# Optimization experiments

Hardware: AMD Instinct MI355X
Metric: run time of the kernel (lower is better)

Reference implementation:

```python
import jax, jax.numpy as jnp
import numpy as np

EPS = 1e-6
TEMP = 1.0
L = 64  # shapelet_len


def _znorm(a):
    # z-normalize over last axis, population std, clamped by EPS (matches torch unbiased=False + clamp_min)
    mean = a.mean(axis=-1, keepdims=True)
    std = jnp.maximum(a.std(axis=-1, keepdims=True), EPS)
    return (a - mean) / std


def setup_inputs() -> dict:
    key = jax.random.key(0)
    k1, k2 = jax.random.split(key)
    bs, T, C, P = 32, 8192, 1, 64
    x = jax.random.normal(k1, (bs, T, C), dtype=jnp.float32)
    shapelets = jax.random.normal(k2, (P, C, L), dtype=jnp.float32)
    return {"x": x, "shapelets": shapelets}


def reference(x, shapelets):
    # x: [bs, T, C]; shapelets: [P, C, L]
    bs, T, C = x.shape
    P = shapelets.shape[0]
    x_ct = jnp.transpose(x, (0, 2, 1))  # [bs, C, T]
    Tp = T - L + 1
    # sliding windows: [bs, C, T', L]
    idx = jnp.arange(Tp)[:, None] + jnp.arange(L)[None, :]
    w = x_ct[:, :, idx]
    # z-normalize windows and shapelets over the length axis
    w = _znorm(w)
    s = _znorm(shapelets)
    # squared euclidean distance via expansion ||w||^2 - 2 w.s + ||s||^2 (sum over C and L)
    w2 = jnp.sum(w * w, axis=(1, 3))          # [bs, T']
    s2 = jnp.sum(s * s, axis=(1, 2))          # [P]
    dot = jnp.einsum('bctl,pcl->btp', w, s)   # [bs, T', P]
    dist2 = w2[:, :, None] + s2[None, None, :] - 2.0 * dot
    temp = max(TEMP, EPS)
    act = jnp.exp(-dist2 / temp)              # [bs, T', P]
    # center-pad to length T: left = L//2, right = T - (T' + left)
    left = L // 2
    right = max(0, T - (Tp + left))
    act_full = jnp.pad(act, ((0, 0), (left, right), (0, 0)))
    return act_full[:, :T, :]
```

## Files before the change

### kernel.cpp

```cpp
#include <hip/hip_runtime.h>
#include <math.h>

#define T_LEN 8192
#define EPSF  1e-6f

typedef __attribute__((ext_vector_type(8))) short short8;
typedef __attribute__((ext_vector_type(4))) float float4v;

__global__ __launch_bounds__(256, 4) void shapelet_fused(
        const float* __restrict__ x,
        const float* __restrict__ sh,
        float* __restrict__ out) {
    __shared__ short8 BfragH[8][64];
    __shared__ short8 BfragL[8][64];
    __shared__ __align__(16) float xs[320];
    __shared__ float4 lstat[256];
    __shared__ __align__(16) float lsum[64];
    __shared__ __align__(16) float ls2[64];

    const int tid  = threadIdx.x;
    const int lane = tid & 63;
    const int wave = tid >> 6;
    const int n    = lane & 15;
    const int quad = lane >> 4;

    const int super = blockIdx.x & 31;
    const int b     = blockIdx.x >> 5;
    const int t0    = super << 8;

    if (tid < 64) {
        const int p = tid;
        const int pt_p = p & 3;
        const int n_p  = p >> 2;

        float S[64];
        const float4* s4 = (const float4*)(sh + (size_t)p * 64);
#pragma unroll
        for (int i = 0; i < 16; ++i) {
            float4 v = s4[i];
            S[4 * i + 0] = v.x;
            S[4 * i + 1] = v.y;
            S[4 * i + 2] = v.z;
            S[4 * i + 3] = v.w;
        }

        float s1 = 0.f;
#pragma unroll
        for (int l = 0; l < 64; ++l) s1 += S[l];
        float mu = s1 * (1.f / 64.f);
        float sq = 0.f;
#pragma unroll
        for (int l = 0; l < 64; ++l) { float d = S[l] - mu; sq = fmaf(d, d, sq); }
        float sd  = fmaxf(sqrtf(sq * (1.f / 64.f)), EPSF);
        float inv = 1.f / sd;
        float ssum = 0.f, ss2 = 0.f;

        unsigned* BH = (unsigned*)BfragH;
        unsigned* BL = (unsigned*)BfragL;
#pragma unroll
        for (int l2 = 0; l2 < 32; ++l2) {
            const int k = 2 * l2;
            unsigned pk_h, pk_l;
            {
                float v = S[k];
                float s = (v - mu) * inv;
                unsigned ub = __float_as_uint(s);
                float hi = __uint_as_float(ub & 0xFFFF0000u);
                float lo = s - hi;
                unsigned lb = __float_as_uint(lo) & 0xFFFF0000u;
                pk_h = ub >> 16;
                pk_l = lb >> 16;
                float eff = hi + __uint_as_float(lb);
                ssum += eff;
                ss2  = fmaf(eff, eff, ss2);
            }
            {
                float v = S[k + 1];
                float s = (v - mu) * inv;
                unsigned ub = __float_as_uint(s);
                float hi = __uint_as_float(ub & 0xFFFF0000u);
                float lo = s - hi;
                unsigned lb = __float_as_uint(lo) & 0xFFFF0000u;
                pk_h |= (ub & 0xFFFF0000u);
                pk_l |= lb;
                float eff = hi + __uint_as_float(lb);
                ssum += eff;
                ss2  = fmaf(eff, eff, ss2);
            }
            const int f  = (pt_p << 1) + (k >> 5);
            const int li = (((k >> 3) & 3) << 4) + n_p;
            const int di = (((f << 6) + li) << 2) + ((k & 7) >> 1);
            BH[di] = pk_h;
            BL[di] = pk_l;
        }
        lsum[p] = ssum;
        ls2[p]  = ss2;
    } else if (tid < 144) {
        const int i = tid - 64;
        int g0 = t0 - 32 + (i << 2);
        float4 v;
        if (g0 >= 0 && g0 + 3 < T_LEN) {
            v = *(const float4*)(x + (size_t)b * T_LEN + g0);
        } else {
            float* vp = (float*)&v;
#pragma unroll
            for (int e = 0; e < 4; ++e) {
                int g = g0 + e;
                vp[e] = ((unsigned)g < (unsigned)T_LEN) ? x[(size_t)b * T_LEN + g] : 0.f;
            }
        }
        *(float4*)&xs[i << 2] = v;
    }
    __syncthreads();

    {
        const int r = tid;
        float s1 = 0.f, sq = 0.f;
#pragma unroll
        for (int l = 0; l < 64; ++l) {
            float v = xs[r + l];
            s1 += v; sq = fmaf(v, v, sq);
        }
        float mu  = s1 * (1.f / 64.f);
        float var = fmaxf(sq * (1.f / 64.f) - mu * mu, 0.f);
        float sd  = fmaxf(sqrtf(var), EPSF);
        float inv = 1.f / sd;
        float4 st;
        st.x = mu;
        st.y = inv;
        st.z = 64.f * var * inv * inv;
        st.w = 0.f;
        lstat[r] = st;
    }
    const float4 sm4 = *(const float4*)&lsum[n << 2];
    const float4 sv4 = *(const float4*)&ls2[n << 2];
    __syncthreads();

    const short8* BH8 = (const short8*)BfragH;
    const short8* BL8 = (const short8*)BfragL;

#pragma unroll
    for (int u = 0; u < 4; ++u) {
        const int abase = (u << 6) + (wave << 4) + n + (quad << 3);
        short8 Ah[2], Al[2];
#pragma unroll
        for (int h = 0; h < 2; ++h) {
#pragma unroll
            for (int j = 0; j < 8; ++j) {
                float v = xs[abase + h * 32 + j];
                unsigned ub = __float_as_uint(v);
                unsigned hb = ub & 0xFFFF0000u;
                float lo = v - __uint_as_float(hb);
                Ah[h][j] = (short)(ub >> 16);
                Al[h][j] = (short)(__float_as_uint(lo) >> 16);
            }
        }

        float4v acc[4];
#pragma unroll
        for (int pt = 0; pt < 4; ++pt) {
            unsigned off = ((unsigned)(pt << 1) << 6) + (unsigned)lane;
            asm volatile("" : "+v"(off));
            short8 bh0 = BH8[off];
            short8 bh1 = BH8[off + 64];
            short8 bl0 = BL8[off];
            short8 bl1 = BL8[off + 64];

            float4v a = {0.f, 0.f, 0.f, 0.f};
            a = __builtin_amdgcn_mfma_f32_16x16x32_bf16(Ah[0], bh0, a, 0, 0, 0);
            a = __builtin_amdgcn_mfma_f32_16x16x32_bf16(Ah[0], bl0, a, 0, 0, 0);
            a = __builtin_amdgcn_mfma_f32_16x16x32_bf16(Al[0], bh0, a, 0, 0, 0);
            a = __builtin_amdgcn_mfma_f32_16x16x32_bf16(Ah[1], bh1, a, 0, 0, 0);
            a = __builtin_amdgcn_mfma_f32_16x16x32_bf16(Ah[1], bl1, a, 0, 0, 0);
            a = __builtin_amdgcn_mfma_f32_16x16x32_bf16(Al[1], bh1, a, 0, 0, 0);
            acc[pt] = a;
        }

#pragma unroll
        for (int r = 0; r < 4; ++r) {
            int tl = (u << 6) + (wave << 4) + (quad << 2) + r;
            int tg = t0 + tl;
            bool valid = (tg >= 32) && (tg <= 8160);
            float4 st = lstat[tl];
            float mu  = st.x;
            float inv = st.y;
            float w2  = st.z;
            float d0 = (acc[0][r] - mu * sm4.x) * inv;
            float d1 = (acc[1][r] - mu * sm4.y) * inv;
            float d2 = (acc[2][r] - mu * sm4.z) * inv;
            float d3 = (acc[3][r] - mu * sm4.w) * inv;
            float4 o;
            o.x = valid ? __expf(-(w2 + sv4.x - 2.f * d0)) : 0.f;
            o.y = valid ? __expf(-(w2 + sv4.y - 2.f * d1)) : 0.f;
            o.z = valid ? __expf(-(w2 + sv4.z - 2.f * d2)) : 0.f;
            o.w = valid ? __expf(-(w2 + sv4.w - 2.f * d3)) : 0.f;
            *(float4*)(out + (((size_t)(b * T_LEN + tg)) << 6) + (n << 2)) = o;
        }
    }
}

extern "C" void kernel_launch(void* const* d_in, const int* in_sizes, int n_in,
                              void* d_out, int out_size, void* d_ws, size_t ws_size,
                              hipStream_t stream) {
    const float* x  = (const float*)d_in[0];
    const float* sh = (const float*)d_in[1];
    float* out = (float*)d_out;

    shapelet_fused<<<32 * 32, 256, 0, stream>>>(x, sh, out);
}
```

Before: 83.88 us.

## Halve per-block time tile, double grid, and cut register pressure for occupancy

Each block now covers 128 time steps instead of 256, so the grid doubles to 2048 blocks and the launch bound asks for 8 waves per SIMD. The shapelet prologue rereads global memory instead of keeping a 64-float register array. The A-fragment bf16 split uses perm-based packing, and the MFMA loop is reordered to process one K-half at a time with accumulators held across halves. The goal is lower VGPR use and better latency hiding, at the cost of redoing the shapelet normalization and B-fragment build in twice as many blocks.

```diff
diff --git a/kernel.cpp b/kernel.cpp
--- a/kernel.cpp
+++ b/kernel.cpp
@@ -7,14 +7,14 @@
 typedef __attribute__((ext_vector_type(8))) short short8;
 typedef __attribute__((ext_vector_type(4))) float float4v;
 
-__global__ __launch_bounds__(256, 4) void shapelet_fused(
+__global__ __launch_bounds__(256, 8) void shapelet_fused(
         const float* __restrict__ x,
         const float* __restrict__ sh,
         float* __restrict__ out) {
     __shared__ short8 BfragH[8][64];
     __shared__ short8 BfragL[8][64];
-    __shared__ __align__(16) float xs[320];
-    __shared__ float4 lstat[256];
+    __shared__ __align__(16) float xs[192];
+    __shared__ float4 lstat[128];
     __shared__ __align__(16) float lsum[64];
     __shared__ __align__(16) float ls2[64];
 
@@ -24,78 +24,83 @@
     const int n    = lane & 15;
     const int quad = lane >> 4;
 
-    const int super = blockIdx.x & 31;
-    const int b     = blockIdx.x >> 5;
-    const int t0    = super << 8;
+    const int super = blockIdx.x & 63;
+    const int b     = blockIdx.x >> 6;
+    const int t0    = super << 7;
 
     if (tid < 64) {
         const int p = tid;
         const int pt_p = p & 3;
         const int n_p  = p >> 2;
-
-        float S[64];
         const float4* s4 = (const float4*)(sh + (size_t)p * 64);
+
+        float s1 = 0.f;
 #pragma unroll
         for (int i = 0; i < 16; ++i) {
             float4 v = s4[i];
-            S[4 * i + 0] = v.x;
-            S[4 * i + 1] = v.y;
-            S[4 * i + 2] = v.z;
-            S[4 * i + 3] = v.w;
-        }
-
-        float s1 = 0.f;
-#pragma unroll
-        for (int l = 0; l < 64; ++l) s1 += S[l];
+            s1 += v.x; s1 += v.y; s1 += v.z; s1 += v.w;
+        }
         float mu = s1 * (1.f / 64.f);
+
         float sq = 0.f;
 #pragma unroll
-        for (int l = 0; l < 64; ++l) { float d = S[l] - mu; sq = fmaf(d, d, sq); }
+        for (int i = 0; i < 16; ++i) {
+            float4 v = s4[i];
+            float d0 = v.x - mu; sq = fmaf(d0, d0, sq);
+            float d1 = v.y - mu; sq = fmaf(d1, d1, sq);
+            float d2 = v.z - mu; sq = fmaf(d2, d2, sq);
+            float d3 = v.w - mu; sq = fmaf(d3, d3, sq);
+        }
         float sd  = fmaxf(sqrtf(sq * (1.f / 64.f)), EPSF);
         float inv = 1.f / sd;
+
         float ssum = 0.f, ss2 = 0.f;
-
         unsigned* BH = (unsigned*)BfragH;
         unsigned* BL = (unsigned*)BfragL;
 #pragma unroll
-        for (int l2 = 0; l2 < 32; ++l2) {
-            const int k = 2 * l2;
-            unsigned pk_h, pk_l;
-            {
-                float v = S[k];
-                float s = (v - mu) * inv;
-                unsigned ub = __float_as_uint(s);
-                float hi = __uint_as_float(ub & 0xFFFF0000u);
-                float lo = s - hi;
-                unsigned lb = __float_as_uint(lo) & 0xFFFF0000u;
-                pk_h = ub >> 16;
-                pk_l = lb >> 16;
-                float eff = hi + __uint_as_float(lb);
-                ssum += eff;
-                ss2  = fmaf(eff, eff, ss2);
-            }
-            {
-                float v = S[k + 1];
-                float s = (v - mu) * inv;
-                unsigned ub = __float_as_uint(s);
-                float hi = __uint_as_float(ub & 0xFFFF0000u);
-                float lo = s - hi;
-                unsigned lb = __float_as_uint(lo) & 0xFFFF0000u;
-                pk_h |= (ub & 0xFFFF0000u);
-                pk_l |= lb;
-                float eff = hi + __uint_as_float(lb);
-                ssum += eff;
-                ss2  = fmaf(eff, eff, ss2);
-            }
-            const int f  = (pt_p << 1) + (k >> 5);
-            const int li = (((k >> 3) & 3) << 4) + n_p;
-            const int di = (((f << 6) + li) << 2) + ((k & 7) >> 1);
-            BH[di] = pk_h;
-            BL[di] = pk_l;
+        for (int i = 0; i < 16; ++i) {
+            float4 v4 = s4[i];
+            const float el[4] = { v4.x, v4.y, v4.z, v4.w };
+#pragma unroll
+            for (int half = 0; half < 2; ++half) {
+                const int k = 4 * i + 2 * half;
+                unsigned pk_h, pk_l;
+                {
+                    float v = el[2 * half];
+                    float s = (v - mu) * inv;
+                    unsigned ub = __float_as_uint(s);
+                    float hi = __uint_as_float(ub & 0xFFFF0000u);
+                    float lo = s - hi;
+                    unsigned lb = __float_as_uint(lo) & 0xFFFF0000u;
+                    pk_h = ub >> 16;
+                    pk_l = lb >> 16;
+                    float eff = hi + __uint_as_float(lb);
+                    ssum += eff;
+                    ss2  = fmaf(eff, eff, ss2);
+                }
+                {
+                    float v = el[2 * half + 1];
+                    float s = (v - mu) * inv;
+                    unsigned ub = __float_as_uint(s);
+                    float hi = __uint_as_float(ub & 0xFFFF0000u);
+                    float lo = s - hi;
+                    unsigned lb = __float_as_uint(lo) & 0xFFFF0000u;
+                    pk_h |= (ub & 0xFFFF0000u);
+                    pk_l |= lb;
+                    float eff = hi + __uint_as_float(lb);
+                    ssum += eff;
+                    ss2  = fmaf(eff, eff, ss2);
+                }
+                const int f  = (pt_p << 1) + (k >> 5);
+                const int li = (((k >> 3) & 3) << 4) + n_p;
+                const int di = (((f << 6) + li) << 2) + ((k & 7) >> 1);
+                BH[di] = pk_h;
+                BL[di] = pk_l;
+            }
         }
         lsum[p] = ssum;
         ls2[p]  = ss2;
-    } else if (tid < 144) {
+    } else if (tid < 112) {
         const int i = tid - 64;
         int g0 = t0 - 32 + (i << 2);
         float4 v;
@@ -113,7 +118,7 @@
     }
     __syncthreads();
 
-    {
+    if (tid < 128) {
         const int r = tid;
         float s1 = 0.f, sq = 0.f;
 #pragma unroll
@@ -140,40 +145,41 @@
     const short8* BL8 = (const short8*)BfragL;
 
 #pragma unroll
-    for (int u = 0; u < 4; ++u) {
+    for (int u = 0; u < 2; ++u) {
         const int abase = (u << 6) + (wave << 4) + n + (quad << 3);
-        short8 Ah[2], Al[2];
+
+        float4v acc[4] = { {0.f,0.f,0.f,0.f}, {0.f,0.f,0.f,0.f},
+                           {0.f,0.f,0.f,0.f}, {0.f,0.f,0.f,0.f} };
 #pragma unroll
         for (int h = 0; h < 2; ++h) {
-#pragma unroll
-            for (int j = 0; j < 8; ++j) {
-                float v = xs[abase + h * 32 + j];
-                unsigned ub = __float_as_uint(v);
-                unsigned hb = ub & 0xFFFF0000u;
-                float lo = v - __uint_as_float(hb);
-                Ah[h][j] = (short)(ub >> 16);
-                Al[h][j] = (short)(__float_as_uint(lo) >> 16);
-            }
-        }
-
-        float4v acc[4];
-#pragma unroll
-        for (int pt = 0; pt < 4; ++pt) {
-            unsigned off = ((unsigned)(pt << 1) << 6) + (unsigned)lane;
-            asm volatile("" : "+v"(off));
-            short8 bh0 = BH8[off];
-            short8 bh1 = BH8[off + 64];
-            short8 bl0 = BL8[off];
-            short8 bl1 = BL8[off + 64];
-
-            float4v a = {0.f, 0.f, 0.f, 0.f};
-            a = __builtin_amdgcn_mfma_f32_16x16x32_bf16(Ah[0], bh0, a, 0, 0, 0);
-            a = __builtin_amdgcn_mfma_f32_16x16x32_bf16(Ah[0], bl0, a, 0, 0, 0);
-            a = __builtin_amdgcn_mfma_f32_16x16x32_bf16(Al[0], bh0, a, 0, 0, 0);
-            a = __builtin_amdgcn_mfma_f32_16x16x32_bf16(Ah[1], bh1, a, 0, 0, 0);
-            a = __builtin_amdgcn_mfma_f32_16x16x32_bf16(Ah[1], bl1, a, 0, 0, 0);
-            a = __builtin_amdgcn_mfma_f32_16x16x32_bf16(Al[1], bh1, a, 0, 0, 0);
-            acc[pt] = a;
+            union { unsigned w[4]; short8 v; } ph, pl;
+#pragma unroll
+            for (int j2 = 0; j2 < 4; ++j2) {
+                float v0 = xs[abase + h * 32 + 2 * j2];
+                float v1 = xs[abase + h * 32 + 2 * j2 + 1];
+                unsigned u0 = __float_as_uint(v0);
+                unsigned u1 = __float_as_uint(v1);
+                float l0 = v0 - __uint_as_float(u0 & 0xFFFF0000u);
+                float l1 = v1 - __uint_as_float(u1 & 0xFFFF0000u);
+                ph.w[j2] = __builtin_amdgcn_perm(u1, u0, 0x07060302u);
+                pl.w[j2] = __builtin_amdgcn_perm(__float_as_uint(l1),
+                                                 __float_as_uint(l0), 0x07060302u);
+            }
+            const short8 Ah = ph.v;
+            const short8 Al = pl.v;
+
+#pragma unroll
+            for (int pt = 0; pt < 4; ++pt) {
+                unsigned off = ((unsigned)(((pt << 1) + h)) << 6) + (unsigned)lane;
+                asm volatile("" : "+v"(off));
+                short8 bh = BH8[off];
+                short8 bl = BL8[off];
+                float4v a = acc[pt];
+                a = __builtin_amdgcn_mfma_f32_16x16x32_bf16(Ah, bh, a, 0, 0, 0);
+                a = __builtin_amdgcn_mfma_f32_16x16x32_bf16(Ah, bl, a, 0, 0, 0);
+                a = __builtin_amdgcn_mfma_f32_16x16x32_bf16(Al, bh, a, 0, 0, 0);
+                acc[pt] = a;
+            }
         }
 
 #pragma unroll
@@ -206,5 +212,5 @@
     const float* sh = (const float*)d_in[1];
     float* out = (float*)d_out;
 
-    shapelet_fused<<<32 * 32, 256, 0, stream>>>(x, sh, out);
+    shapelet_fused<<<32 * 64, 256, 0, stream>>>(x, sh, out);
 }
```

Result: slower. 109.2 us (+30.2%).
